# Kernel optimization log

Measured on AMD Instinct MI355X. Metric: run time of the kernel, lower is better.

The kernel has to match this reference:

```python
import jax, jax.numpy as jnp
import numpy as np

OUT_FEATURES = 4096
IN_FEATURES = 4096
GROUP_SIZE = 16


def setup_inputs() -> dict:
    key = jax.random.key(0)
    k1, k2, k3, k4 = jax.random.split(key, 4)
    n_groups = OUT_FEATURES * IN_FEATURES // GROUP_SIZE
    x = jax.random.normal(k1, (8, 2048, IN_FEATURES), dtype=jnp.float32)
    weight_q = jax.random.randint(k2, (n_groups, GROUP_SIZE), 0, 16, dtype=jnp.int32).astype(jnp.int8)
    weight_norm = jax.random.uniform(k3, (n_groups, 1), dtype=jnp.float32).astype(jnp.float16)
    bias = jax.random.normal(k4, (OUT_FEATURES,), dtype=jnp.float32)
    return {"x": x, "weight_q": weight_q, "weight_norm": weight_norm, "bias": bias}


def reference(x, weight_q, weight_norm, bias):
    # block dequant: (q/15) * per-group scale, then reshape to [out, in]
    w = (weight_q.astype(jnp.float32) / 15.0) * weight_norm.astype(jnp.float32)
    w = w.reshape(OUT_FEATURES, IN_FEATURES)
    # F.linear: x @ w^T + bias
    return jnp.einsum('bsi,oi->bso', x, w) + bias
```

## Files before the change

kernel.cpp:

```cpp
#include <hip/hip_runtime.h>

#define MDIM 16384
#define NDIM 4096
#define KDIM 4096
#define NT   64

typedef unsigned short u16;
typedef unsigned int   u32;
typedef __attribute__((ext_vector_type(8))) short bh8;
typedef __attribute__((ext_vector_type(4))) float f32x4;
typedef __attribute__((ext_vector_type(4))) int   i32x4;

__device__ __forceinline__ u16 f2bf(float f) {
  u32 u = __builtin_bit_cast(u32, f);
  u = (u + 0x7fffu + ((u >> 16) & 1u)) >> 16;
  return (u16)u;
}

__device__ __forceinline__ void gld16(const void* g, const void* lds) {
  __builtin_amdgcn_global_load_lds((const __attribute__((address_space(1))) u32*)g,
                                   (__attribute__((address_space(3))) u32*)lds, 16, 0, 0);
}

__global__ void cvt_x(const float* __restrict__ x, u16* __restrict__ xb) {
  size_t i = ((size_t)blockIdx.x * 256 + threadIdx.x) * 8;
  f32x4 a = *(const f32x4*)(x + i);
  f32x4 b = *(const f32x4*)(x + i + 4);
  bh8 o;
  o[0] = (short)f2bf(a[0]); o[1] = (short)f2bf(a[1]);
  o[2] = (short)f2bf(a[2]); o[3] = (short)f2bf(a[3]);
  o[4] = (short)f2bf(b[0]); o[5] = (short)f2bf(b[1]);
  o[6] = (short)f2bf(b[2]); o[7] = (short)f2bf(b[3]);
  *(bh8*)(xb + i) = o;
}

__global__ void deq_w(const int* __restrict__ qi, const void* __restrict__ nrm,
                      u16* __restrict__ wb) {
  __shared__ int s_q8, s_n32;
  if (threadIdx.x == 0) {
    int packed = 0;
    for (int t = 0; t < 64; ++t) { unsigned v = (unsigned)qi[t]; if (v > 15u) packed = 1; }
    int n32 = 0;
    const u16* h = (const u16*)nrm;
    for (int t = 0; t < 64; ++t) { u16 b = h[t]; if (b < 0x8000u && b > 0x3C00u) n32 = 1; }
    s_q8 = packed; s_n32 = n32;
  }
  __syncthreads();
  const bool q8 = (s_q8 != 0), n32 = (s_n32 != 0);

  int g = blockIdx.x * 256 + threadIdx.x;
  float s;
  if (n32) s = ((const float*)nrm)[g] * (1.0f / 15.0f);
  else {
    u16 hb = ((const u16*)nrm)[g];
    s = (float)__builtin_bit_cast(_Float16, hb) * (1.0f / 15.0f);
  }
  float q[16];
  if (q8) {
    i32x4 v = *(const i32x4*)((const unsigned char*)qi + (size_t)g * 16);
#pragma unroll
    for (int k = 0; k < 4; ++k) {
      int word = v[k];
      q[k*4+0] = (float)(word & 255);        q[k*4+1] = (float)((word >> 8) & 255);
      q[k*4+2] = (float)((word >> 16) & 255); q[k*4+3] = (float)((word >> 24) & 255);
    }
  } else {
    const i32x4* p = (const i32x4*)(qi + (size_t)g * 16);
#pragma unroll
    for (int k = 0; k < 4; ++k) {
      i32x4 v = p[k];
      q[k*4+0] = (float)v[0]; q[k*4+1] = (float)v[1];
      q[k*4+2] = (float)v[2]; q[k*4+3] = (float)v[3];
    }
  }
  bh8 o0, o1;
#pragma unroll
  for (int j = 0; j < 8; ++j) o0[j] = (short)f2bf(q[j] * s);
#pragma unroll
  for (int j = 0; j < 8; ++j) o1[j] = (short)f2bf(q[8 + j] * s);
  *(bh8*)(wb + (size_t)g * 16) = o0;
  *(bh8*)(wb + (size_t)g * 16 + 8) = o1;
}

__global__ __launch_bounds__(512, 2) void gemm8(const u16* __restrict__ A,
                                                const u16* __restrict__ B,
                                                const float* __restrict__ bias,
                                                float* __restrict__ out) {
  __shared__ u16 lds[65536];
  const int tid = threadIdx.x;
  const int w = tid >> 6, l = tid & 63;
  const int wm = w >> 2, wn = w & 3;

  int bid = blockIdx.x;
  int wg = (bid & 7) * 128 + (bid >> 3);
  const int bm = wg >> 4;
  const int bn = wg & 15;

  const int cs8  = ((l & 7) ^ (l >> 3)) * 8;
  const u16* aSrc = A + (size_t)(bm * 256 + w * 32 + (l >> 3)) * 4096 + cs8;
  const u16* bSrc = B + (size_t)(bn * 256 + w * 32 + (l >> 3)) * 4096 + cs8;

  const int fr  = (l & 15) * 64;
  const int sz0 = ((l >> 4) ^ (l & 7)) * 8;
  const int sz1 = ((4 + (l >> 4)) ^ (l & 7)) * 8;

  f32x4 acc[8][4];
#pragma unroll
  for (int mi = 0; mi < 8; ++mi)
#pragma unroll
    for (int ni = 0; ni < 4; ++ni) acc[mi][ni] = (f32x4){0.f, 0.f, 0.f, 0.f};

  bh8 aX[2][2], aY[2][2];
  bh8 bf_[4][2];

  auto STG = [&](int op, int h, int kt) {
    const u16* s = (op ? bSrc : aSrc) + h * 65536 + kt * 64;
    int d = (op ? 32768 : 0) + ((kt & 1) * 2 + h) * 8192 + w * 1024;
    gld16(s,         &lds[d]);
    gld16(s + 32768, &lds[d + 512]);
  };
  auto RDA = [&](int buf, int mb, bh8 (&aa)[2][2]) {
#pragma unroll
    for (int q = 0; q < 2; ++q) {
      int base = (buf * 2 + q) * 8192 + (wm * 4 + mb) * 1024 + fr;
      aa[q][0] = *(const bh8*)&lds[base + sz0];
      aa[q][1] = *(const bh8*)&lds[base + sz1];
    }
  };
  auto RDB = [&](int buf) {
#pragma unroll
    for (int r = 0; r < 4; ++r) {
      int base = 32768 + (buf * 2 + (r & 1)) * 8192 + (wn * 2 + (r >> 1)) * 1024 + fr;
      bf_[r][0] = *(const bh8*)&lds[base + sz0];
      bf_[r][1] = *(const bh8*)&lds[base + sz1];
    }
  };
  auto MMB = [&](int mb, bh8 (&aa)[2][2]) {
    __builtin_amdgcn_s_setprio(1);
#pragma unroll
    for (int kk = 0; kk < 2; ++kk)
#pragma unroll
      for (int q = 0; q < 2; ++q)
#pragma unroll
        for (int r = 0; r < 4; ++r)
          acc[mb*2+q][r] = __builtin_amdgcn_mfma_f32_16x16x32_bf16(
              aa[q][kk], bf_[r][kk], acc[mb*2+q][r], 0, 0, 0);
    __builtin_amdgcn_s_setprio(0);
  };

#define BAR1 asm volatile("" ::: "memory"); __builtin_amdgcn_s_barrier(); \
             asm volatile("" ::: "memory");
#define BAR2 asm volatile("" ::: "memory"); __builtin_amdgcn_s_barrier();
#define SBAR __builtin_amdgcn_sched_barrier(0);

  STG(1, 0, 0); STG(1, 1, 0); STG(0, 0, 0); STG(0, 1, 0);
  STG(1, 0, 1); STG(1, 1, 1); STG(0, 0, 1); STG(0, 1, 1);
  asm volatile("s_waitcnt vmcnt(8)");
  BAR1;
  RDA(0, 0, aX); RDB(0);

#pragma unroll 1
  for (int i = 0; i < NT / 2 - 1; ++i) {
    const int c = 2 * i + 2, d = 2 * i + 3;
    RDA(0, 1, aY);
    BAR1; MMB(0, aX); BAR2;
    RDA(0, 2, aX); STG(1, 0, c);
    BAR1; MMB(1, aY); BAR2;
    RDA(0, 3, aY); STG(1, 1, c);
    BAR1; MMB(2, aX); BAR2;
    STG(0, 0, c); asm volatile("s_waitcnt vmcnt(6)");
    BAR1; RDA(1, 0, aX); MMB(3, aY); SBAR; RDB(1); BAR2;
    RDA(1, 1, aY); STG(0, 1, c);
    BAR1; MMB(0, aX); BAR2;
    RDA(1, 2, aX); STG(1, 0, d);
    BAR1; MMB(1, aY); BAR2;
    RDA(1, 3, aY); STG(1, 1, d);
    BAR1; MMB(2, aX); BAR2;
    STG(0, 0, d); STG(0, 1, d); asm volatile("s_waitcnt vmcnt(8)");
    BAR1; RDA(0, 0, aX); MMB(3, aY); SBAR; RDB(0); BAR2;
  }
  RDA(0, 1, aY);
  BAR1; MMB(0, aX); BAR2;
  RDA(0, 2, aX);
  BAR1; MMB(1, aY); BAR2;
  RDA(0, 3, aY);
  BAR1; MMB(2, aX); BAR2;
  asm volatile("s_waitcnt vmcnt(0)");
  BAR1; RDA(1, 0, aX); MMB(3, aY); SBAR; RDB(1); BAR2;
  RDA(1, 1, aY);
  BAR1; MMB(0, aX); BAR2;
  RDA(1, 2, aX);
  BAR1; MMB(1, aY); BAR2;
  RDA(1, 3, aY);
  BAR1; MMB(2, aX); BAR2;
  BAR1; MMB(3, aY);
#undef BAR1
#undef BAR2
#undef SBAR

  const int col0 = bn * 256 + wn * 64 + (l & 15);
  const int row0 = bm * 256 + wm * 128 + (l >> 4) * 4;
#pragma unroll
  for (int ni = 0; ni < 4; ++ni) {
    float bv = bias[col0 + ni * 16];
#pragma unroll
    for (int mi = 0; mi < 8; ++mi) {
      size_t base = (size_t)(row0 + mi * 16) * 4096 + (size_t)(col0 + ni * 16);
#pragma unroll
      for (int rr = 0; rr < 4; ++rr)
        out[base + (size_t)rr * 4096] = acc[mi][ni][rr] + bv;
    }
  }
}

__global__ __launch_bounds__(512, 2) void gemm_fb(const float* __restrict__ Af32,
                                                  const u16* __restrict__ Wbf,
                                                  const float* __restrict__ bias,
                                                  float* __restrict__ out) {
  __shared__ u16 lds[65536];
  const int tid = threadIdx.x;
  const int w = tid >> 6, l = tid & 63;
  const int wm = w >> 2, wn = w & 3;
  int bid = blockIdx.x;
  int wg = (bid & 7) * 128 + (bid >> 3);
  const int bm = wg >> 4, bn = wg & 15;

  int srcOffB[4], srcOffA32[4], dstSwzA[4];
#pragma unroll
  for (int j = 0; j < 4; ++j) {
    int ci = (w * 4 + j) * 64 + l;
    int r = ci >> 3, c = ci & 7;
    int cs = c ^ (r & 7);
    srcOffB[j]   = (bn * 256 + r) * 4096 + cs * 8;
    srcOffA32[j] = (bm * 256 + r) * 4096 + c * 8;
    dstSwzA[j]   = r * 64 + cs * 8;
  }
  const int ar = wm * 128 + (l & 15);
  const int br = wn * 64 + (l & 15);
  const int swz0 = (((l >> 4) + 0) ^ (l & 7)) * 8;
  const int swz1 = (((l >> 4) + 4) ^ (l & 7)) * 8;
  const int aoff0 = ar * 64 + swz0, aoff1 = ar * 64 + swz1;
  const int boff0 = 32768 + br * 64 + swz0, boff1 = 32768 + br * 64 + swz1;

  f32x4 acc[8][4];
#pragma unroll
  for (int mi = 0; mi < 8; ++mi)
#pragma unroll
    for (int ni = 0; ni < 4; ++ni) acc[mi][ni] = (f32x4){0.f, 0.f, 0.f, 0.f};

  auto STAGE = [&](int bufb, int kt) {
    const int kof = kt * 64;
#pragma unroll
    for (int j = 0; j < 4; ++j) {
      gld16(Wbf + srcOffB[j] + kof, &lds[32768 + bufb * 16384 + (w * 4 + j) * 512]);
      const float* p = Af32 + srcOffA32[j] + kof;
      f32x4 v0 = *(const f32x4*)p;
      f32x4 v1 = *(const f32x4*)(p + 4);
      bh8 o;
      o[0] = (short)f2bf(v0[0]); o[1] = (short)f2bf(v0[1]);
      o[2] = (short)f2bf(v0[2]); o[3] = (short)f2bf(v0[3]);
      o[4] = (short)f2bf(v1[0]); o[5] = (short)f2bf(v1[1]);
      o[6] = (short)f2bf(v1[2]); o[7] = (short)f2bf(v1[3]);
      *(bh8*)&lds[bufb * 16384 + dstSwzA[j]] = o;
    }
  };
  auto COMPUTE = [&](int bufb) {
    const int ab = bufb * 16384;
#pragma unroll
    for (int kk = 0; kk < 2; ++kk) {
      const int ao = ab + (kk ? aoff1 : aoff0);
      const int bo = ab + (kk ? boff1 : boff0);
      bh8 afr[8], bfr[4];
#pragma unroll
      for (int mi = 0; mi < 8; ++mi) afr[mi] = *(const bh8*)&lds[ao + mi * 1024];
#pragma unroll
      for (int ni = 0; ni < 4; ++ni) bfr[ni] = *(const bh8*)&lds[bo + ni * 1024];
#pragma unroll
      for (int mi = 0; mi < 8; ++mi)
#pragma unroll
        for (int ni = 0; ni < 4; ++ni)
          acc[mi][ni] = __builtin_amdgcn_mfma_f32_16x16x32_bf16(afr[mi], bfr[ni],
                                                                acc[mi][ni], 0, 0, 0);
    }
  };

  int buf = 0;
  STAGE(0, 0);
  __syncthreads();
  for (int kt = 0; kt < NT - 1; ++kt) {
    STAGE(buf ^ 1, kt + 1);
    COMPUTE(buf);
    __syncthreads();
    buf ^= 1;
  }
  COMPUTE(buf);

  const int col0 = bn * 256 + wn * 64 + (l & 15);
  const int row0 = bm * 256 + wm * 128 + (l >> 4) * 4;
#pragma unroll
  for (int ni = 0; ni < 4; ++ni) {
    float bv = bias[col0 + ni * 16];
#pragma unroll
    for (int mi = 0; mi < 8; ++mi) {
      size_t base = (size_t)(row0 + mi * 16) * 4096 + (size_t)(col0 + ni * 16);
#pragma unroll
      for (int rr = 0; rr < 4; ++rr)
        out[base + (size_t)rr * 4096] = acc[mi][ni][rr] + bv;
    }
  }
}

extern "C" void kernel_launch(void* const* d_in, const int* in_sizes, int n_in,
                              void* d_out, int out_size, void* d_ws, size_t ws_size,
                              hipStream_t stream) {
  const float* x    = (const float*)d_in[0];
  const int*   wq   = (const int*)d_in[1];
  const void*  wn   = d_in[2];
  const float* bias = (const float*)d_in[3];
  float*       out  = (float*)d_out;

  const size_t needA = (size_t)MDIM * KDIM * 2;
  const size_t needW = (size_t)NDIM * KDIM * 2;

  if (ws_size >= needA + needW) {
    u16* xbf = (u16*)d_ws;
    u16* wbf = (u16*)((char*)d_ws + needA);
    cvt_x<<<dim3(32768), dim3(256), 0, stream>>>(x, xbf);
    deq_w<<<dim3(4096), dim3(256), 0, stream>>>(wq, wn, wbf);
    gemm8<<<dim3(1024), dim3(512), 0, stream>>>(xbf, wbf, bias, out);
  } else if (ws_size >= needW) {
    u16* wbf = (u16*)d_ws;
    deq_w<<<dim3(4096), dim3(256), 0, stream>>>(wq, wn, wbf);
    gemm_fb<<<dim3(1024), dim3(512), 0, stream>>>(x, wbf, bias, out);
  }
}
```

Measured before the change: 538.7 us.

## Restructure GEMM main loop to halve barriers and overlap LDS reads with MFMAs

Reorganizes the software-pipelined main loop so each barrier-bracketed phase runs two MFMA blocks, each followed by the LDS fragment read for the next step, instead of one MFMA block per barrier pair. Global-to-LDS stages are grouped in pairs with a single waitcnt per phase. This cuts barrier count per iteration and aims to hide LDS read latency behind matrix work. It risks changing register pressure and LDS hazard ordering, since reads now sit inside the same barrier region as the compute.

```diff
diff --git a/kernel.cpp b/kernel.cpp
--- a/kernel.cpp
+++ b/kernel.cpp
@@ -157,43 +157,48 @@
   STG(1, 0, 1); STG(1, 1, 1); STG(0, 0, 1); STG(0, 1, 1);
   asm volatile("s_waitcnt vmcnt(8)");
   BAR1;
-  RDA(0, 0, aX); RDB(0);
+  RDA(0, 0, aX); RDB(0); RDA(0, 1, aY);
 
 #pragma unroll 1
   for (int i = 0; i < NT / 2 - 1; ++i) {
     const int c = 2 * i + 2, d = 2 * i + 3;
-    RDA(0, 1, aY);
-    BAR1; MMB(0, aX); BAR2;
-    RDA(0, 2, aX); STG(1, 0, c);
-    BAR1; MMB(1, aY); BAR2;
-    RDA(0, 3, aY); STG(1, 1, c);
-    BAR1; MMB(2, aX); BAR2;
-    STG(0, 0, c); asm volatile("s_waitcnt vmcnt(6)");
-    BAR1; RDA(1, 0, aX); MMB(3, aY); SBAR; RDB(1); BAR2;
-    RDA(1, 1, aY); STG(0, 1, c);
-    BAR1; MMB(0, aX); BAR2;
-    RDA(1, 2, aX); STG(1, 0, d);
-    BAR1; MMB(1, aY); BAR2;
-    RDA(1, 3, aY); STG(1, 1, d);
-    BAR1; MMB(2, aX); BAR2;
+    STG(1, 0, c); STG(1, 1, c);
+    BAR1;
+    MMB(0, aX); SBAR; RDA(0, 2, aX);
+    MMB(1, aY); SBAR; RDA(0, 3, aY);
+    BAR2;
+    STG(0, 0, c); STG(0, 1, c); asm volatile("s_waitcnt vmcnt(8)");
+    BAR1;
+    MMB(2, aX); SBAR; RDA(1, 0, aX);
+    MMB(3, aY); SBAR; RDB(1); RDA(1, 1, aY);
+    BAR2;
+    STG(1, 0, d); STG(1, 1, d);
+    BAR1;
+    MMB(0, aX); SBAR; RDA(1, 2, aX);
+    MMB(1, aY); SBAR; RDA(1, 3, aY);
+    BAR2;
     STG(0, 0, d); STG(0, 1, d); asm volatile("s_waitcnt vmcnt(8)");
-    BAR1; RDA(0, 0, aX); MMB(3, aY); SBAR; RDB(0); BAR2;
-  }
-  RDA(0, 1, aY);
-  BAR1; MMB(0, aX); BAR2;
-  RDA(0, 2, aX);
-  BAR1; MMB(1, aY); BAR2;
-  RDA(0, 3, aY);
-  BAR1; MMB(2, aX); BAR2;
+    BAR1;
+    MMB(2, aX); SBAR; RDA(0, 0, aX);
+    MMB(3, aY); SBAR; RDB(0); RDA(0, 1, aY);
+    BAR2;
+  }
+  BAR1;
+  MMB(0, aX); SBAR; RDA(0, 2, aX);
+  MMB(1, aY); SBAR; RDA(0, 3, aY);
+  BAR2;
   asm volatile("s_waitcnt vmcnt(0)");
-  BAR1; RDA(1, 0, aX); MMB(3, aY); SBAR; RDB(1); BAR2;
-  RDA(1, 1, aY);
-  BAR1; MMB(0, aX); BAR2;
-  RDA(1, 2, aX);
-  BAR1; MMB(1, aY); BAR2;
-  RDA(1, 3, aY);
-  BAR1; MMB(2, aX); BAR2;
-  BAR1; MMB(3, aY);
+  BAR1;
+  MMB(2, aX); SBAR; RDA(1, 0, aX);
+  MMB(3, aY); SBAR; RDB(1); RDA(1, 1, aY);
+  BAR2;
+  BAR1;
+  MMB(0, aX); SBAR; RDA(1, 2, aX);
+  MMB(1, aY); SBAR; RDA(1, 3, aY);
+  BAR2;
+  BAR1;
+  MMB(2, aX);
+  MMB(3, aY);
 #undef BAR1
 #undef BAR2
 #undef SBAR
```

New measurement: 543.5 us. Within noise of the previous version (+0.9%).
